# Kernel optimization log

Hardware: AMD Instinct MI355X
Metric: run time of the kernel (lower is better)

The kernel has to match this reference:

```python
import jax, jax.numpy as jnp
import numpy as np

NUM_PL, NUM_TR, NUM_AR = 50000, 100000, 10000
HID, FEAT, NUM_LAYERS = 64, 128, 2


def setup_inputs() -> dict:
    key = jax.random.key(0)
    ks = jax.random.split(key, 16)
    inp = {
        'track_x': jax.random.normal(ks[0], (NUM_TR, FEAT), dtype=jnp.float32),
        'pl_tr_src': jax.random.randint(ks[1], (2000000,), 0, NUM_PL, dtype=jnp.int32),
        'pl_tr_dst': jax.random.randint(ks[2], (2000000,), 0, NUM_TR, dtype=jnp.int32),
        'tr_ar_src': jax.random.randint(ks[3], (100000,), 0, NUM_TR, dtype=jnp.int32),
        'tr_ar_dst': jax.random.randint(ks[4], (100000,), 0, NUM_AR, dtype=jnp.int32),
        # learned parameters
        'playlist_emb': jax.random.normal(ks[5], (NUM_PL, HID), dtype=jnp.float32),
        'artist_emb': jax.random.normal(ks[6], (NUM_AR, HID), dtype=jnp.float32),
        'track_W': jax.random.normal(ks[7], (HID, FEAT), dtype=jnp.float32) / np.sqrt(FEAT),
        'track_b': jnp.zeros((HID,), dtype=jnp.float32),
        'type_emb': jax.random.normal(ks[8], (3, HID), dtype=jnp.float32),
        # SAGEConv params per layer: lin_l (neighbor, with bias), lin_r (root, no bias)
        'conv_Wl': jax.random.normal(ks[9], (NUM_LAYERS, HID, HID), dtype=jnp.float32) / np.sqrt(HID),
        'conv_bl': jnp.zeros((NUM_LAYERS, HID), dtype=jnp.float32),
        'conv_Wr': jax.random.normal(ks[10], (NUM_LAYERS, HID, HID), dtype=jnp.float32) / np.sqrt(HID),
    }
    return inp


def reference(track_x, pl_tr_src, pl_tr_dst, tr_ar_src, tr_ar_dst,
              playlist_emb, artist_emb, track_W, track_b, type_emb,
              conv_Wl, conv_bl, conv_Wr):
    off_tr = NUM_PL
    off_ar = NUM_PL + NUM_TR
    N = NUM_PL + NUM_TR + NUM_AR

    # node features: [playlist_emb; track_lin(track_x); artist_emb] + type_emb[type]
    x_tr = track_x @ track_W.T + track_b
    x = jnp.concatenate([playlist_emb, x_tr, artist_emb], axis=0)
    type_ids = jnp.concatenate([
        jnp.zeros((NUM_PL,), jnp.int32),
        jnp.ones((NUM_TR,), jnp.int32),
        jnp.full((NUM_AR,), 2, jnp.int32)])
    x = x + type_emb[type_ids]

    # combined edge index: pl->tr, tr->pl, tr->ar, ar->tr (global node ids)
    pl = pl_tr_src
    tr1 = pl_tr_dst + off_tr
    tr2 = tr_ar_src + off_tr
    ar = tr_ar_dst + off_ar
    src = jnp.concatenate([pl, tr1, tr2, ar])
    dst = jnp.concatenate([tr1, pl, ar, tr2])

    # mean-aggregation degrees (clamped to avoid div by 0)
    deg = jax.ops.segment_sum(jnp.ones_like(src, dtype=x.dtype), dst, num_segments=N)
    deg = jnp.maximum(deg, 1.0)[:, None]

    for l in range(NUM_LAYERS):
        agg = jax.ops.segment_sum(x[src], dst, num_segments=N) / deg  # mean over neighbors
        x = jax.nn.relu(agg @ conv_Wl[l].T + conv_bl[l] + x @ conv_Wr[l].T)

    return (x[:off_tr], x[off_tr:off_ar], x[off_ar:])
```

## Files before the change

kernel.cpp:

```cpp
#include <hip/hip_runtime.h>

#define NUM_PL 50000
#define NUM_TR 100000
#define NUM_AR 10000
#define NN     160000
#define HID    64
#define FEAT   128
#define E_PLTR 2000000
#define E_TRAR 100000
#define E_TOT  4200000
#define OFF_TR 50000
#define OFF_AR 150000

#define BIN_CHUNK 8192
#define NBLK_BIN  513
#define NBUCK     625
#define TABW      626
#define PKD_CAP   (NBLK_BIN * BIN_CHUNK)

#define WSTR 65

#define SCAP 11520

__device__ __forceinline__ float h2f(ushort u) {
  _Float16 h = __builtin_bit_cast(_Float16, u);
  return (float)h;
}
__device__ __forceinline__ ushort f2h(float f) {
  _Float16 h = (_Float16)f;
  return __builtin_bit_cast(ushort, h);
}

__device__ __forceinline__ void fmix_lo(float& a, uint u) {
  asm("v_fma_mix_f32 %0, %1, 1.0, %0 op_sel_hi:[1,0,0]"
      : "+v"(a) : "v"(u));
}
__device__ __forceinline__ void fmix_hi(float& a, uint u) {
  asm("v_fma_mix_f32 %0, %1, 1.0, %0 op_sel:[1,0,0] op_sel_hi:[1,0,0]"
      : "+v"(a) : "v"(u));
}
__device__ __forceinline__ void acc_h4(float4& a, ushort4 u) {
  uint2 w = __builtin_bit_cast(uint2, u);
  fmix_lo(a.x, w.x); fmix_hi(a.y, w.x);
  fmix_lo(a.z, w.y); fmix_hi(a.w, w.y);
}

__device__ __forceinline__ void edge_sd(
    int e, const int* __restrict__ pls, const int* __restrict__ pld,
    const int* __restrict__ tas, const int* __restrict__ tad, int& s, int& d) {
  if (e < E_PLTR)                   { s = pls[e];               d = pld[e] + OFF_TR; }
  else if (e < 2 * E_PLTR)          { int i = e - E_PLTR;
                                      s = pld[i] + OFF_TR;      d = pls[i]; }
  else if (e < 2 * E_PLTR + E_TRAR) { int i = e - 2 * E_PLTR;
                                      s = tas[i] + OFF_TR;      d = tad[i] + OFF_AR; }
  else                              { int i = e - 2 * E_PLTR - E_TRAR;
                                      s = tad[i] + OFF_AR;      d = tas[i] + OFF_TR; }
}

__global__ __launch_bounds__(256) void k_init_emb(
    const float* __restrict__ pl_emb, const float* __restrict__ ar_emb,
    const float* __restrict__ type_emb, float* __restrict__ x,
    ushort* __restrict__ xh) {
  int tid = blockIdx.x * 256 + threadIdx.x;
  int f = tid & (HID - 1);
  if (tid < NUM_PL * HID) {
    float v = pl_emb[tid] + type_emb[f];
    x[tid] = v;
    xh[tid] = f2h(v);
  } else {
    int idx = tid - NUM_PL * HID;
    if (idx < NUM_AR * HID) {
      float v = ar_emb[idx] + type_emb[2 * HID + f];
      x[OFF_AR * HID + idx] = v;
      xh[OFF_AR * HID + idx] = f2h(v);
    }
  }
}

__global__ __launch_bounds__(256) void k_track_lin(
    const float* __restrict__ tx, const float* __restrict__ W,
    const float* __restrict__ b, const float* __restrict__ type_emb,
    float* __restrict__ x, ushort* __restrict__ xh) {
  __shared__ float WS[FEAT * 65];
  __shared__ float bs[HID];
  int t = threadIdx.x;
  for (int idx = t; idx < HID * FEAT; idx += 256) {
    int j = idx >> 7, k = idx & (FEAT - 1);
    WS[k * 65 + j] = W[idx];
  }
  if (t < HID) bs[t] = b[t] + type_emb[HID + t];
  __syncthreads();

  int j  = t & 63;
  int wv = __builtin_amdgcn_readfirstlane(t >> 6);
  int row0 = blockIdx.x * 32 + wv * 8;
  const float* xr = tx + (size_t)row0 * FEAT;

  float acc[8] = {0.f, 0.f, 0.f, 0.f, 0.f, 0.f, 0.f, 0.f};
#pragma unroll 4
  for (int k = 0; k < FEAT; ++k) {
    float w = WS[k * 65 + j];
#pragma unroll
    for (int r = 0; r < 8; ++r)
      acc[r] += xr[r * FEAT + k] * w;
  }
#pragma unroll
  for (int r = 0; r < 8; ++r) {
    float v = acc[r] + bs[j];
    x[(OFF_TR + row0 + r) * HID + j] = v;
    xh[(OFF_TR + row0 + r) * HID + j] = f2h(v);
  }
}

__global__ __launch_bounds__(256) void k_bin(
    const int* __restrict__ pls, const int* __restrict__ pld,
    const int* __restrict__ tas, const int* __restrict__ tad,
    int* __restrict__ pkd, int* __restrict__ tab, int* __restrict__ btot) {
  __shared__ int hist[TABW];
  __shared__ int offs[TABW];
  __shared__ int scanbuf[256];
  int t = threadIdx.x;
  int blk = blockIdx.x;
  int e0 = blk * BIN_CHUNK;
  int e1 = e0 + BIN_CHUNK; if (e1 > E_TOT) e1 = E_TOT;

  for (int i = t; i < TABW; i += 256) hist[i] = 0;
  __syncthreads();

  for (int e = e0 + t; e < e1; e += 256) {
    int s, d; edge_sd(e, pls, pld, tas, tad, s, d);
    int b = min(max(d >> 8, 0), NBUCK - 1);
    atomicAdd(&hist[b], 1);
  }
  __syncthreads();

  int i0 = 3 * t, i1 = 3 * t + 1, i2 = 3 * t + 2;
  int h0 = (i0 < NBUCK) ? hist[i0] : 0;
  int h1 = (i1 < NBUCK) ? hist[i1] : 0;
  int h2 = (i2 < NBUCK) ? hist[i2] : 0;
  if (i0 < NBUCK && h0) atomicAdd(&btot[i0], h0);
  if (i1 < NBUCK && h1) atomicAdd(&btot[i1], h1);
  if (i2 < NBUCK && h2) atomicAdd(&btot[i2], h2);
  int lsum = h0 + h1 + h2;
  scanbuf[t] = lsum;
  __syncthreads();
  int incl = lsum;
#pragma unroll
  for (int off = 1; off < 256; off <<= 1) {
    int add = (t >= off) ? scanbuf[t - off] : 0;
    __syncthreads();
    incl += add;
    scanbuf[t] = incl;
    __syncthreads();
  }
  int base = incl - lsum;
  if (i0 < TABW) offs[i0] = base;
  if (i1 < TABW) offs[i1] = base + h0;
  if (i2 < TABW) offs[i2] = base + h0 + h1;
  __syncthreads();

  for (int i = t; i < TABW; i += 256) tab[blk * TABW + i] = e0 + offs[i];
  for (int i = t; i < NBUCK; i += 256) hist[i] = offs[i];
  __syncthreads();

  for (int e = e0 + t; e < e1; e += 256) {
    int s, d; edge_sd(e, pls, pld, tas, tad, s, d);
    int b = min(max(d >> 8, 0), NBUCK - 1);
    int pos = atomicAdd(&hist[b], 1);
    int idx = min(max(e0 + pos, 0), PKD_CAP - 1);
    pkd[idx] = ((d & 255) << 18) | s;
  }
}

__global__ __launch_bounds__(1024) void k_bscan(int* __restrict__ btot) {
  __shared__ int s[1024];
  int t = threadIdx.x;
  int val = (t < NBUCK) ? btot[t] : 0;
  s[t] = val;
  __syncthreads();
  int incl = val;
#pragma unroll
  for (int off = 1; off < 1024; off <<= 1) {
    int add = (t >= off) ? s[t - off] : 0;
    __syncthreads();
    incl += add;
    s[t] = incl;
    __syncthreads();
  }
  if (t < NBUCK) btot[t] = incl - val;
}

__global__ __launch_bounds__(256) void k_fill3(
    const int* __restrict__ tab, const int* __restrict__ pkd,
    const int* __restrict__ btot, int* __restrict__ rowptr,
    int* __restrict__ col) {
  __shared__ int stage[SCAP];
  __shared__ int cnt[256];
  __shared__ int scanbuf[256];
  __shared__ int validS;
  int t = threadIdx.x;
  int b = blockIdx.x;

  int s0a = tab[t * TABW + b],         s1a = tab[t * TABW + b + 1];
  int s0b = tab[(t + 256) * TABW + b], s1b = tab[(t + 256) * TABW + b + 1];
  int s0c = 0, s1c = 0;
  if (t + 512 < NBLK_BIN) {
    s0c = tab[(t + 512) * TABW + b];   s1c = tab[(t + 512) * TABW + b + 1];
  }
  s0a = min(max(s0a, 0), PKD_CAP); s1a = min(max(s1a, s0a), PKD_CAP);
  s0b = min(max(s0b, 0), PKD_CAP); s1b = min(max(s1b, s0b), PKD_CAP);
  s0c = min(max(s0c, 0), PKD_CAP); s1c = min(max(s1c, s0c), PKD_CAP);
  int len = (s1a - s0a) + (s1b - s0b) + (s1c - s0c);

  cnt[t] = 0;
  if (t == 0) validS = 0x7fffffff;
  scanbuf[t] = len;
  __syncthreads();
  int incl = len;
#pragma unroll
  for (int off = 1; off < 256; off <<= 1) {
    int add = (t >= off) ? scanbuf[t - off] : 0;
    __syncthreads();
    incl += add;
    scanbuf[t] = incl;
    __syncthreads();
  }
  int base = incl - len;
  int totalE = scanbuf[255];
  bool fits = (base + len <= SCAP);
  if (!fits) atomicMin(&validS, base);
  __syncthreads();
  int valid = min(validS, totalE);

  int off = base;
  for (int i = s0a; i < s1a; ++i) {
    int pk = pkd[i];
    atomicAdd(&cnt[(pk >> 18) & 255], 1);
    if (fits) stage[off++] = pk;
  }
  for (int i = s0b; i < s1b; ++i) {
    int pk = pkd[i];
    atomicAdd(&cnt[(pk >> 18) & 255], 1);
    if (fits) stage[off++] = pk;
  }
  for (int i = s0c; i < s1c; ++i) {
    int pk = pkd[i];
    atomicAdd(&cnt[(pk >> 18) & 255], 1);
    if (fits) stage[off++] = pk;
  }
  __syncthreads();

  int val = cnt[t];
  scanbuf[t] = val;
  __syncthreads();
  incl = val;
#pragma unroll
  for (int off2 = 1; off2 < 256; off2 <<= 1) {
    int add = (t >= off2) ? scanbuf[t - off2] : 0;
    __syncthreads();
    incl += add;
    scanbuf[t] = incl;
    __syncthreads();
  }
  int rp = btot[b] + incl - val;
  rowptr[(b << 8) + t] = rp;
  if (b == NBUCK - 1 && t == 255) rowptr[NN] = E_TOT;
  __syncthreads();
  cnt[t] = rp;
  __syncthreads();

  for (int i = t; i < valid; i += 256) {
    int pk = stage[i];
    int pos = atomicAdd(&cnt[(pk >> 18) & 255], 1);
    pos = min(max(pos, 0), E_TOT - 1);
    col[pos] = pk & 0x3FFFF;
  }
  if (!fits) {
    for (int i = s0a; i < s1a; ++i) {
      int pk = pkd[i];
      int pos = atomicAdd(&cnt[(pk >> 18) & 255], 1);
      pos = min(max(pos, 0), E_TOT - 1);
      col[pos] = pk & 0x3FFFF;
    }
    for (int i = s0b; i < s1b; ++i) {
      int pk = pkd[i];
      int pos = atomicAdd(&cnt[(pk >> 18) & 255], 1);
      pos = min(max(pos, 0), E_TOT - 1);
      col[pos] = pk & 0x3FFFF;
    }
    for (int i = s0c; i < s1c; ++i) {
      int pk = pkd[i];
      int pos = atomicAdd(&cnt[(pk >> 18) & 255], 1);
      pos = min(max(pos, 0), E_TOT - 1);
      col[pos] = pk & 0x3FFFF;
    }
  }
}

__global__ __launch_bounds__(1024, 8) void k_gather_update(
    const int* __restrict__ rowptr, const int* __restrict__ col,
    const ushort* __restrict__ xh,
    const float* __restrict__ Wl, const float* __restrict__ bl,
    const float* __restrict__ Wr,
    ushort* __restrict__ xnh, float* __restrict__ xnf) {
  __shared__ float WlS[HID * WSTR];
  __shared__ float WrS[HID * WSTR];
  __shared__ float bs[HID];
  __shared__ __align__(16) float rowS[16][4][2 * HID];
  int t = threadIdx.x;
  for (int idx = t; idx < HID * HID; idx += 1024) {
    int j = idx >> 6, k = idx & 63;
    WlS[k * WSTR + j] = Wl[idx];
    WrS[k * WSTR + j] = Wr[idx];
  }
  if (t < HID) bs[t] = bl[t];
  __syncthreads();

  int lane = t & 63;
  int wv = t >> 6;
  int r = lane >> 4;
  int c = lane & 15;
  const ushort4* xh4 = (const ushort4*)xh;
  int nbase = (blockIdx.x * 16 + wv) * 4;

  for (int it = 0; it < 4; ++it) {
    int n = nbase + it;
    int rp0 = rowptr[n], rp1 = rowptr[n + 1];

    ushort4 ru;
    if (r == 0) ru = xh4[n * 16 + c];

    float4 a0 = {0.f, 0.f, 0.f, 0.f};
    float4 a1 = {0.f, 0.f, 0.f, 0.f};
    float4 a2 = {0.f, 0.f, 0.f, 0.f};
    float4 a3 = {0.f, 0.f, 0.f, 0.f};
    int base = rp0;
    for (; base + 16 <= rp1; base += 16) {
      int s0 = col[base + r];
      int s1 = col[base + 4 + r];
      int s2 = col[base + 8 + r];
      int s3 = col[base + 12 + r];
      ushort4 u0 = xh4[s0 * 16 + c];
      ushort4 u1 = xh4[s1 * 16 + c];
      ushort4 u2 = xh4[s2 * 16 + c];
      ushort4 u3 = xh4[s3 * 16 + c];
      acc_h4(a0, u0);
      acc_h4(a1, u1);
      acc_h4(a2, u2);
      acc_h4(a3, u3);
    }
    if (base + 4 <= rp1) {
      int s0 = col[base + r];
      acc_h4(a0, xh4[s0 * 16 + c]);
      base += 4;
    }
    if (base + 4 <= rp1) {
      int s1 = col[base + r];
      acc_h4(a1, xh4[s1 * 16 + c]);
      base += 4;
    }
    if (base + 4 <= rp1) {
      int s2 = col[base + r];
      acc_h4(a2, xh4[s2 * 16 + c]);
      base += 4;
    }
    if (base + r < rp1) {
      int s3 = col[base + r];
      acc_h4(a3, xh4[s3 * 16 + c]);
    }
    float4 a;
    a.x = (a0.x + a1.x) + (a2.x + a3.x);
    a.y = (a0.y + a1.y) + (a2.y + a3.y);
    a.z = (a0.z + a1.z) + (a2.z + a3.z);
    a.w = (a0.w + a1.w) + (a2.w + a3.w);
    a.x += __shfl_xor(a.x, 16); a.y += __shfl_xor(a.y, 16);
    a.z += __shfl_xor(a.z, 16); a.w += __shfl_xor(a.w, 16);
    a.x += __shfl_xor(a.x, 32); a.y += __shfl_xor(a.y, 32);
    a.z += __shfl_xor(a.z, 32); a.w += __shfl_xor(a.w, 32);

    if (r == 0) {
      float id = 1.0f / (float)max(rp1 - rp0, 1);
      float4 o;
      o.x = a.x * id; o.y = a.y * id; o.z = a.z * id; o.w = a.w * id;
      float4 rootf;
      rootf.x = h2f(ru.x); rootf.y = h2f(ru.y);
      rootf.z = h2f(ru.z); rootf.w = h2f(ru.w);
      ((float4*)&rowS[wv][it][0])[c] = o;
      ((float4*)&rowS[wv][it][0])[16 + c] = rootf;
    }
  }

  asm volatile("s_waitcnt lgkmcnt(0)" ::: "memory");
  __builtin_amdgcn_sched_barrier(0);

  const float4* row0 = (const float4*)&rowS[wv][0][0];
  const float4* row1 = (const float4*)&rowS[wv][1][0];
  const float4* row2 = (const float4*)&rowS[wv][2][0];
  const float4* row3 = (const float4*)&rowS[wv][3][0];
  float acc0 = 0.f, acc1 = 0.f, acc2 = 0.f, acc3 = 0.f;
#pragma unroll 2
  for (int k4 = 0; k4 < 16; ++k4) {
    float4 g0 = row0[k4], t0 = row0[16 + k4];
    float4 g1 = row1[k4], t1 = row1[16 + k4];
    float4 g2 = row2[k4], t2 = row2[16 + k4];
    float4 g3 = row3[k4], t3 = row3[16 + k4];
    int k = k4 * 4;
    float wl0 = WlS[(k + 0) * WSTR + lane], wr0 = WrS[(k + 0) * WSTR + lane];
    float wl1 = WlS[(k + 1) * WSTR + lane], wr1 = WrS[(k + 1) * WSTR + lane];
    float wl2 = WlS[(k + 2) * WSTR + lane], wr2 = WrS[(k + 2) * WSTR + lane];
    float wl3 = WlS[(k + 3) * WSTR + lane], wr3 = WrS[(k + 3) * WSTR + lane];
    acc0 += g0.x * wl0 + g0.y * wl1 + g0.z * wl2 + g0.w * wl3
          + t0.x * wr0 + t0.y * wr1 + t0.z * wr2 + t0.w * wr3;
    acc1 += g1.x * wl0 + g1.y * wl1 + g1.z * wl2 + g1.w * wl3
          + t1.x * wr0 + t1.y * wr1 + t1.z * wr2 + t1.w * wr3;
    acc2 += g2.x * wl0 + g2.y * wl1 + g2.z * wl2 + g2.w * wl3
          + t2.x * wr0 + t2.y * wr1 + t2.z * wr2 + t2.w * wr3;
    acc3 += g3.x * wl0 + g3.y * wl1 + g3.z * wl2 + g3.w * wl3
          + t3.x * wr0 + t3.y * wr1 + t3.z * wr2 + t3.w * wr3;
  }
  float bias = bs[lane];
  float o0 = fmaxf(acc0 + bias, 0.f);
  float o1 = fmaxf(acc1 + bias, 0.f);
  float o2 = fmaxf(acc2 + bias, 0.f);
  float o3 = fmaxf(acc3 + bias, 0.f);
  if (xnf) {
    xnf[(nbase + 0) * HID + lane] = o0;
    xnf[(nbase + 1) * HID + lane] = o1;
    xnf[(nbase + 2) * HID + lane] = o2;
    xnf[(nbase + 3) * HID + lane] = o3;
  } else {
    xnh[(nbase + 0) * HID + lane] = f2h(o0);
    xnh[(nbase + 1) * HID + lane] = f2h(o1);
    xnh[(nbase + 2) * HID + lane] = f2h(o2);
    xnh[(nbase + 3) * HID + lane] = f2h(o3);
  }
}

extern "C" void kernel_launch(void* const* d_in, const int* in_sizes, int n_in,
                              void* d_out, int out_size, void* d_ws, size_t ws_size,
                              hipStream_t stream) {
  const float* track_x  = (const float*)d_in[0];
  const int*   pl_tr_s  = (const int*)d_in[1];
  const int*   pl_tr_d  = (const int*)d_in[2];
  const int*   tr_ar_s  = (const int*)d_in[3];
  const int*   tr_ar_d  = (const int*)d_in[4];
  const float* pl_emb   = (const float*)d_in[5];
  const float* ar_emb   = (const float*)d_in[6];
  const float* track_W  = (const float*)d_in[7];
  const float* track_b  = (const float*)d_in[8];
  const float* type_emb = (const float*)d_in[9];
  const float* conv_Wl  = (const float*)d_in[10];
  const float* conv_bl  = (const float*)d_in[11];
  const float* conv_Wr  = (const float*)d_in[12];

  float* x = (float*)d_out;

  char* w = (char*)d_ws;
  ushort* xh1   = (ushort*)w;
  int*   pkd    = (int*)w;
  int*   tab    = (int*)(w + (size_t)PKD_CAP * 4);
  w += (size_t)NN * HID * 2;
  ushort* xh0   = (ushort*)w; w += (size_t)NN * HID * 2;
  int*   col    = (int*)w;    w += (size_t)E_TOT * 4;
  int*   rowptr = (int*)w;    w += (size_t)(NN + 1) * 4;
  int*   btot   = (int*)w;

  hipMemsetAsync(btot, 0, NBUCK * sizeof(int), stream);

  k_init_emb<<<(NUM_PL + NUM_AR) * HID / 256, 256, 0, stream>>>(
      pl_emb, ar_emb, type_emb, x, xh0);
  k_track_lin<<<NUM_TR / 32, 256, 0, stream>>>(
      track_x, track_W, track_b, type_emb, x, xh0);

  k_bin<<<NBLK_BIN, 256, 0, stream>>>(
      pl_tr_s, pl_tr_d, tr_ar_s, tr_ar_d, pkd, tab, btot);
  k_bscan<<<1, 1024, 0, stream>>>(btot);
  k_fill3<<<NBUCK, 256, 0, stream>>>(tab, pkd, btot, rowptr, col);

  k_gather_update<<<NN / 64, 1024, 0, stream>>>(
      rowptr, col, xh0, conv_Wl, conv_bl, conv_Wr, xh1, nullptr);
  k_gather_update<<<NN / 64, 1024, 0, stream>>>(
      rowptr, col, xh1, conv_Wl + HID * HID, conv_bl + HID,
      conv_Wr + HID * HID, xh0 , x);
}
```

Baseline: 620.5 us.

## Cache packed edges in LDS during binning and halve bin chunk size

The binning kernel now stores each edge's packed value and bucket id in shared memory during the histogram pass, so the scatter pass no longer re-reads and re-decodes the edge arrays from global memory. The bin chunk is halved so these per-block LDS buffers fit, which doubles the number of binning blocks. The fill kernel is generalized to loop over a variable number of source blocks per thread. Costs are more per-block tables to read in the fill kernel, shorter contiguous runs per segment, and extra LDS use in the binning kernel.

```diff
diff --git a/kernel.cpp b/kernel.cpp
--- a/kernel.cpp
+++ b/kernel.cpp
@@ -12,8 +12,8 @@
 #define OFF_TR 50000
 #define OFF_AR 150000
 
-#define BIN_CHUNK 8192
-#define NBLK_BIN  513
+#define BIN_CHUNK 4096
+#define NBLK_BIN  1026
 #define NBUCK     625
 #define TABW      626
 #define PKD_CAP   (NBLK_BIN * BIN_CHUNK)
@@ -116,6 +116,8 @@
     const int* __restrict__ pls, const int* __restrict__ pld,
     const int* __restrict__ tas, const int* __restrict__ tad,
     int* __restrict__ pkd, int* __restrict__ tab, int* __restrict__ btot) {
+  __shared__ int    pkL[BIN_CHUNK];
+  __shared__ ushort bL[BIN_CHUNK];
   __shared__ int hist[TABW];
   __shared__ int offs[TABW];
   __shared__ int scanbuf[256];
@@ -130,6 +132,9 @@
   for (int e = e0 + t; e < e1; e += 256) {
     int s, d; edge_sd(e, pls, pld, tas, tad, s, d);
     int b = min(max(d >> 8, 0), NBUCK - 1);
+    int li = e - e0;
+    pkL[li] = ((d & 255) << 18) | s;
+    bL[li] = (ushort)b;
     atomicAdd(&hist[b], 1);
   }
   __syncthreads();
@@ -164,11 +169,11 @@
   __syncthreads();
 
   for (int e = e0 + t; e < e1; e += 256) {
-    int s, d; edge_sd(e, pls, pld, tas, tad, s, d);
-    int b = min(max(d >> 8, 0), NBUCK - 1);
+    int li = e - e0;
+    int b = bL[li];
     int pos = atomicAdd(&hist[b], 1);
     int idx = min(max(e0 + pos, 0), PKD_CAP - 1);
-    pkd[idx] = ((d & 255) << 18) | s;
+    pkd[idx] = pkL[li];
   }
 }
 
@@ -201,16 +206,14 @@
   int t = threadIdx.x;
   int b = blockIdx.x;
 
-  int s0a = tab[t * TABW + b],         s1a = tab[t * TABW + b + 1];
-  int s0b = tab[(t + 256) * TABW + b], s1b = tab[(t + 256) * TABW + b + 1];
-  int s0c = 0, s1c = 0;
-  if (t + 512 < NBLK_BIN) {
-    s0c = tab[(t + 512) * TABW + b];   s1c = tab[(t + 512) * TABW + b + 1];
-  }
-  s0a = min(max(s0a, 0), PKD_CAP); s1a = min(max(s1a, s0a), PKD_CAP);
-  s0b = min(max(s0b, 0), PKD_CAP); s1b = min(max(s1b, s0b), PKD_CAP);
-  s0c = min(max(s0c, 0), PKD_CAP); s1c = min(max(s1c, s0c), PKD_CAP);
-  int len = (s1a - s0a) + (s1b - s0b) + (s1c - s0c);
+  int len = 0;
+  for (int blk = t; blk < NBLK_BIN; blk += 256) {
+    int s0 = tab[blk * TABW + b];
+    int s1 = tab[blk * TABW + b + 1];
+    s0 = min(max(s0, 0), PKD_CAP);
+    s1 = min(max(s1, s0), PKD_CAP);
+    len += s1 - s0;
+  }
 
   cnt[t] = 0;
   if (t == 0) validS = 0x7fffffff;
@@ -233,20 +236,16 @@
   int valid = min(validS, totalE);
 
   int off = base;
-  for (int i = s0a; i < s1a; ++i) {
-    int pk = pkd[i];
-    atomicAdd(&cnt[(pk >> 18) & 255], 1);
-    if (fits) stage[off++] = pk;
-  }
-  for (int i = s0b; i < s1b; ++i) {
-    int pk = pkd[i];
-    atomicAdd(&cnt[(pk >> 18) & 255], 1);
-    if (fits) stage[off++] = pk;
-  }
-  for (int i = s0c; i < s1c; ++i) {
-    int pk = pkd[i];
-    atomicAdd(&cnt[(pk >> 18) & 255], 1);
-    if (fits) stage[off++] = pk;
+  for (int blk = t; blk < NBLK_BIN; blk += 256) {
+    int s0 = tab[blk * TABW + b];
+    int s1 = tab[blk * TABW + b + 1];
+    s0 = min(max(s0, 0), PKD_CAP);
+    s1 = min(max(s1, s0), PKD_CAP);
+    for (int i = s0; i < s1; ++i) {
+      int pk = pkd[i];
+      atomicAdd(&cnt[(pk >> 18) & 255], 1);
+      if (fits) stage[off++] = pk;
+    }
   }
   __syncthreads();
 
@@ -276,23 +275,17 @@
     col[pos] = pk & 0x3FFFF;
   }
   if (!fits) {
-    for (int i = s0a; i < s1a; ++i) {
-      int pk = pkd[i];
-      int pos = atomicAdd(&cnt[(pk >> 18) & 255], 1);
-      pos = min(max(pos, 0), E_TOT - 1);
-      col[pos] = pk & 0x3FFFF;
-    }
-    for (int i = s0b; i < s1b; ++i) {
-      int pk = pkd[i];
-      int pos = atomicAdd(&cnt[(pk >> 18) & 255], 1);
-      pos = min(max(pos, 0), E_TOT - 1);
-      col[pos] = pk & 0x3FFFF;
-    }
-    for (int i = s0c; i < s1c; ++i) {
-      int pk = pkd[i];
-      int pos = atomicAdd(&cnt[(pk >> 18) & 255], 1);
-      pos = min(max(pos, 0), E_TOT - 1);
-      col[pos] = pk & 0x3FFFF;
+    for (int blk = t; blk < NBLK_BIN; blk += 256) {
+      int s0 = tab[blk * TABW + b];
+      int s1 = tab[blk * TABW + b + 1];
+      s0 = min(max(s0, 0), PKD_CAP);
+      s1 = min(max(s1, s0), PKD_CAP);
+      for (int i = s0; i < s1; ++i) {
+        int pk = pkd[i];
+        int pos = atomicAdd(&cnt[(pk >> 18) & 255], 1);
+        pos = min(max(pos, 0), E_TOT - 1);
+        col[pos] = pk & 0x3FFFF;
+      }
     }
   }
 }
```

Result: no change. 615.1 us (-0.9%).
